# Kernel optimization log

Measured on AMD Instinct MI355X. Metric: run time of the kernel, lower is better.

The kernel has to match this reference:

```python
import jax, jax.numpy as jnp
import numpy as np

B = 4096          # trees (characters)
T = 16            # nodes per tree template
VC, VO = 2000, 16
D, H = 256, 512


def _build_trees(rng):
    # template: perfect binary tree depth 3 (nodes 0..14, leaves 7..14) + extra leaf 15
    # node 3 is ternary with third child 15
    left_t = np.full(T, -1, np.int32)
    right_t = np.full(T, -1, np.int32)
    third_t = np.full(T, -1, np.int32)
    for i in range(7):
        left_t[i] = 2 * i + 1
        right_t[i] = 2 * i + 2
    third_t[3] = 15
    off = (np.arange(B, dtype=np.int32) * T)[:, None]
    def shift(t):
        return np.where(t[None, :] >= 0, t[None, :] + off, -1).ravel().astype(np.int32)
    left, right, third = shift(left_t), shift(right_t), shift(third_t)
    comp = np.zeros((B, T), np.int32)
    comp[:, 7:] = rng.integers(1, VC, size=(B, 9))      # leaves get real components
    op = np.zeros((B, T), np.int32)
    op[:, :7] = rng.integers(1, VO, size=(B, 7))        # internal nodes get operators
    lvl0 = (off + np.array([0])).ravel().astype(np.int32)
    lvl1 = (off + np.array([1, 2])).ravel().astype(np.int32)
    lvl2 = (off + np.array([3, 4, 5, 6])).ravel().astype(np.int32)
    return comp.ravel(), op.ravel(), left, right, third, lvl2, lvl1, lvl0


def setup_inputs() -> dict:
    rng = np.random.default_rng(0)
    comp, op, left, right, third, lvl2, lvl1, lvl0 = _build_trees(rng)
    def xavier(fi, fo):
        s = np.sqrt(6.0 / (fi + fo))
        return jnp.asarray(rng.uniform(-s, s, size=(fi, fo)).astype(np.float32))
    comp_table = rng.normal(0, 0.02, size=(VC, D)).astype(np.float32)
    comp_table[0] = 0.0  # padding_idx
    op_table = rng.normal(0, 0.02, size=(VO, D)).astype(np.float32)
    op_table[0] = 0.0
    return {
        'component_ids': jnp.asarray(comp), 'operator_ids': jnp.asarray(op),
        'left_child': jnp.asarray(left), 'right_child': jnp.asarray(right),
        'third_child': jnp.asarray(third),
        'lvl2_idx': jnp.asarray(lvl2), 'lvl1_idx': jnp.asarray(lvl1), 'lvl0_idx': jnp.asarray(lvl0),
        'comp_table': jnp.asarray(comp_table), 'op_table': jnp.asarray(op_table),
        'W1b': xavier(3 * D, H), 'b1b': jnp.zeros((H,), jnp.float32),
        'W2b': xavier(H, D), 'b2b': jnp.zeros((D,), jnp.float32),
        'W1t': xavier(4 * D, H), 'b1t': jnp.zeros((H,), jnp.float32),
        'W2t': xavier(H, D), 'b2t': jnp.zeros((D,), jnp.float32),
        'gamma': jnp.ones((D,), jnp.float32), 'beta': jnp.zeros((D,), jnp.float32),
    }


def _ln(x, gamma, beta, eps=1e-5):
    mu = jnp.mean(x, axis=-1, keepdims=True)
    var = jnp.mean(jnp.square(x - mu), axis=-1, keepdims=True)
    return (x - mu) * jax.lax.rsqrt(var + eps) * gamma + beta


def reference(component_ids, operator_ids, left_child, right_child, third_child,
              lvl2_idx, lvl1_idx, lvl0_idx,
              comp_table, op_table, W1b, b1b, W2b, b2b, W1t, b1t, W2t, b2t,
              gamma, beta):
    node_embeds = comp_table[component_ids]               # [N, D]
    for idx in (lvl2_idx, lvl1_idx, lvl0_idx):            # bottom-up levels
        op_e = op_table[operator_ids[idx]]                # [L, D]
        le = node_embeds[left_child[idx]]
        re = node_embeds[right_child[idx]]
        ti = third_child[idx]
        has3 = (ti >= 0)
        te = node_embeds[jnp.maximum(ti, 0)] * has3[:, None].astype(node_embeds.dtype)
        b_in = jnp.concatenate([op_e, le, re], axis=-1)   # [L, 3D]
        b_out = jax.nn.gelu(b_in @ W1b + b1b, approximate=False) @ W2b + b2b
        t_in = jnp.concatenate([op_e, le, re, te], axis=-1)  # [L, 4D]
        t_out = jax.nn.gelu(t_in @ W1t + b1t, approximate=False) @ W2t + b2t
        new_b = _ln(b_out + le + re, gamma, beta)
        new_t = _ln(t_out + (le + re + te) / 3.0, gamma, beta)
        new = jnp.where(has3[:, None], new_t, new_b)
        node_embeds = node_embeds.at[idx].set(new)
    return node_embeds[lvl0_idx]                          # [B, D] root embeddings (eval: no dropout)
```

## Files before the change

### kernel.cpp

```cpp
#include <hip/hip_runtime.h>

typedef __bf16 bf16_t;
typedef __attribute__((ext_vector_type(8))) __bf16 bf16x8;
typedef __attribute__((ext_vector_type(4))) __bf16 bf16x4;
typedef __attribute__((ext_vector_type(4))) float f32x4;

#define GLL16(gsrc, ldst) __builtin_amdgcn_global_load_lds( \
    (const __attribute__((address_space(1))) void*)(gsrc),  \
    (__attribute__((address_space(3))) void*)(ldst), 16, 0, 0)
#define SBAR() __builtin_amdgcn_s_barrier()
#define SCHED0() __builtin_amdgcn_sched_barrier(0)

__global__ void detect_dtype(const unsigned short* __restrict__ ct, int* __restrict__ flag) {
    if (threadIdx.x == 0 && blockIdx.x == 0) {
        int ok = 1;
        for (int i = 0; i < 16; i++) {
            int e = (ct[256 + i] >> 7) & 0xFF;
            ok &= (e >= 80 && e <= 126) ? 1 : 0;
        }
        *flag = ok;
    }
}

__global__ void prep(const void* __restrict__ op_table, bf16_t* __restrict__ opb,
                     const void* __restrict__ comp_table, bf16_t* __restrict__ ctb,
                     const void* __restrict__ W1b, bf16_t* __restrict__ W1bp,
                     const void* __restrict__ W1t, bf16_t* __restrict__ W1tp,
                     const void* __restrict__ W2b, bf16_t* __restrict__ W2bp,
                     const void* __restrict__ W2t, bf16_t* __restrict__ W2tp,
                     const int* __restrict__ flagp,
                     const int* __restrict__ lvl2, const int* __restrict__ lvl1,
                     const int* __restrict__ lvl0, const int* __restrict__ third,
                     int* __restrict__ lists, int* __restrict__ cnts,
                     int* __restrict__ inv) {
    int b = blockIdx.x, tid = threadIdx.x;
    if (b >= 6624) {
        int r = (b - 6624) * 256 + tid;
        int slot, lr, base_t, base_b;
        const int* lvl;
        if (r < 16384)      { slot = 0; lr = r;         lvl = lvl2; base_t = 0;     base_b = 16384; }
        else if (r < 24576) { slot = 1; lr = r - 16384; lvl = lvl1; base_t = 32768; base_b = 40960; }
        else                { slot = 2; lr = r - 24576; lvl = lvl0; base_t = 49152; base_b = 53248; }
        int node = lvl[lr];
        int tern = third[node] >= 0 ? 1 : 0;
        if (slot == 0)      inv[node] = lr;
        else if (slot == 1) inv[node] = 16384 + lr;

        unsigned long long bt = __ballot(tern);
        unsigned long long bb = __ballot(!tern);
        int lane = tid & 63;
        unsigned long long ltm = (1ull << lane) - 1ull;
        int post = __popcll(bt & ltm), posb = __popcll(bb & ltm);
        int baseT = 0, baseB = 0;
        if (lane == 0) {
            baseT = atomicAdd(&cnts[slot * 2 + 1], __popcll(bt));
            baseB = atomicAdd(&cnts[slot * 2 + 0], __popcll(bb));
        }
        baseT = __shfl(baseT, 0, 64);
        baseB = __shfl(baseB, 0, 64);
        lists[tern ? (base_t + baseT + post) : (base_b + baseB + posb)] = lr;
        return;
    }
    int isbf = *flagp;
    if (b < 16) {
        int i = b * 256 + tid;
        opb[i] = isbf ? ((const bf16_t*)op_table)[i] : (bf16_t)((const float*)op_table)[i];
        return;
    }
    if (b < 2016) {
        int i = (b - 16) * 256 + tid;
        ctb[i] = isbf ? ((const bf16_t*)comp_table)[i] : (bf16_t)((const float*)comp_table)[i];
        return;
    }
    const void* src; bf16_t* dst; int e0, Nmask, Nshift;
    if (b < 3552)      { src = W1b; dst = W1bp; e0 = (b - 2016) * 256; Nmask = 511; Nshift = 9; }
    else if (b < 5600) { src = W1t; dst = W1tp; e0 = (b - 3552) * 256; Nmask = 511; Nshift = 9; }
    else if (b < 6112) { src = W2b; dst = W2bp; e0 = (b - 5600) * 256; Nmask = 255; Nshift = 8; }
    else               { src = W2t; dst = W2tp; e0 = (b - 6112) * 256; Nmask = 255; Nshift = 8; }
    int e = e0 + tid;
    bf16_t v = isbf ? ((const bf16_t*)src)[e] : (bf16_t)((const float*)src)[e];
    int n = e & Nmask, k = e >> Nshift;
    int kc = k >> 5, kl = k & 31;
    int gp = (kl >> 3) ^ ((n >> 1) & 3);
    dst[(size_t)(((kc << Nshift) + n) << 5) + (gp << 3) + (kl & 7)] = v;
}

__device__ __forceinline__ void load8f(const bf16_t* ne2, const void* ct, int isbf,
                                       int invn, int cidn, int q, float* o) {
    if (invn >= 0) {
        bf16x8 v = *(const bf16x8*)(ne2 + (size_t)invn * 256 + q);
        for (int z = 0; z < 8; z++) o[z] = (float)v[z];
    } else if (isbf) {
        bf16x8 v = *(const bf16x8*)((const bf16_t*)ct + (size_t)cidn * 256 + q);
        for (int z = 0; z < 8; z++) o[z] = (float)v[z];
    } else {
        const float* fp = (const float*)ct + (size_t)cidn * 256 + q;
        f32x4 a = *(const f32x4*)fp, b = *(const f32x4*)(fp + 4);
        for (int z = 0; z < 4; z++) { o[z] = a[z]; o[z + 4] = b[z]; }
    }
}

__device__ __forceinline__ float ldparam(const void* p, int i, int isbf) {
    return isbf ? (float)((const bf16_t*)p)[i] : ((const float*)p)[i];
}

__global__ __launch_bounds__(512, 4) void fused_level(
    const int* __restrict__ list_t, const int* __restrict__ list_b,
    const int* __restrict__ cntpair, const int* __restrict__ lvl_idx,
    const int* __restrict__ op_ids, const int* __restrict__ lch,
    const int* __restrict__ rch, const int* __restrict__ tch,
    bf16_t* __restrict__ ne2, const bf16_t* __restrict__ opb,
    const void* __restrict__ ct, const bf16_t* __restrict__ ctb,
    const int* __restrict__ cid, const int* __restrict__ inv,
    const int* __restrict__ flagp,
    const bf16_t* __restrict__ W1tp, const void* __restrict__ b1t,
    const bf16_t* __restrict__ W2tp, const void* __restrict__ b2t,
    const bf16_t* __restrict__ W1bp, const void* __restrict__ b1b,
    const bf16_t* __restrict__ W2bp, const void* __restrict__ b2b,
    const void* __restrict__ gma, const void* __restrict__ bta,
    int slotBase, void* __restrict__ out)
{
    __shared__ __align__(1024) char smem[69632];

    const int tid = threadIdx.x;
    const int w = tid >> 6, lane = tid & 63, cc = lane & 15, qq = lane >> 4;
    const int gx = (cc >> 1) & 3;
    const int e7 = cc & 7;
    const int cnt_t = cntpair[1], cnt_b = cntpair[0];
    const int blocks_t = (cnt_t + 31) >> 5;
    int tern, base, cnt, K1c;
    const int* list;
    const bf16_t *W1p, *W2p;
    const void *b1, *b2;
    if ((int)blockIdx.x < blocks_t) {
        tern = 1; list = list_t; base = blockIdx.x * 32; cnt = cnt_t;
        W1p = W1tp; b1 = b1t; W2p = W2tp; b2 = b2t; K1c = 32;
    } else {
        tern = 0; list = list_b; base = (blockIdx.x - blocks_t) * 32; cnt = cnt_b;
        if (base >= cnt) return;
        W1p = W1bp; b1 = b1b; W2p = W2bp; b2 = b2b; K1c = 24;
    }
    const int act = min(32, cnt - base);
    const int isbf = *flagp;

    int glA = 0, opSA = 0;
    int aInv0 = 0, aInv1 = 0, aInv2 = 0, aCid0 = 0, aCid1 = 0, aCid2 = 0;
    if (tid < 128) {
        int rowA = tid >> 2;
        glA = (tid & 3) ^ ((rowA >> 1) & 3);
        int rA = list[base + min(rowA, act - 1)];
        int nA = lvl_idx[rA];
        opSA = op_ids[nA];
        int a0 = lch[nA], a1 = rch[nA];
        int a2 = tern ? tch[nA] : a0;
        aInv0 = inv[a0]; aInv1 = inv[a1]; aInv2 = inv[a2];
        aCid0 = aInv0 < 0 ? cid[a0] : 0;
        aCid1 = aInv1 < 0 ? cid[a1] : 0;
        aCid2 = aInv2 < 0 ? cid[a2] : 0;
    }

    const int ms = tid >> 4, gs = tid & 15;
    const int lr = list[base + min(ms, act - 1)];
    const int node = lvl_idx[lr];
    const int c0 = lch[node], c1 = rch[node];
    const int c2 = tern ? tch[node] : c0;
    int sInv[3] = {inv[c0], inv[c1], inv[c2]};
    int sCid[3];
    sCid[0] = sInv[0] < 0 ? cid[c0] : 0;
    sCid[1] = sInv[1] < 0 ? cid[c1] : 0;
    sCid[2] = sInv[2] < 0 ? cid[c2] : 0;

    float b2f[2], gf[2], btf[2];
    for (int j = 0; j < 2; j++) {
        int col = (w + 8 * j) * 16 + cc;
        b2f[j] = ldparam(b2, col, isbf);
        gf[j] = ldparam(gma, col, isbf);
        btf[j] = ldparam(bta, col, isbf);
    }

    const f32x4 zf = {0.f, 0.f, 0.f, 0.f};
    f32x4 acc1[2][4];
    for (int m = 0; m < 2; m++) for (int j = 0; j < 4; j++) acc1[m][j] = zf;

#define STAGE1(kc_, bsel_) do {                                                   \
        const char* srcb_ = (const char*)W1p + ((size_t)(kc_) << 15);             \
        char* dstb_ = smem + ((bsel_) << 15);                                     \
        _Pragma("unroll")                                                         \
        for (int i_ = 0; i_ < 4; i_++) {                                          \
            int off_ = ((i_ << 3) + w) << 10;                                     \
            GLL16(srcb_ + off_ + (lane << 4), dstb_ + off_);                      \
        }                                                                         \
        if (w < 2) {                                                              \
            int colg_ = (kc_) * 32 + glA * 8;                                     \
            int piece_ = colg_ >> 8, po_ = colg_ & 255;                           \
            int iv_ = piece_ == 1 ? aInv0 : piece_ == 2 ? aInv1 : aInv2;          \
            int cd_ = piece_ == 1 ? aCid0 : piece_ == 2 ? aCid1 : aCid2;          \
            const bf16_t* s_ = piece_ == 0 ? opb + (size_t)opSA * 256             \
                : (iv_ >= 0 ? ne2 + (size_t)iv_ * 256 : ctb + (size_t)cd_ * 256); \
            GLL16(s_ + po_, smem + 65536 + ((bsel_) << 11) + (w << 10));          \
        }                                                                         \
    } while (0)

    STAGE1(0, 0);
    for (int kc = 0; kc < K1c; kc++) {
        const int cur = kc & 1;
        const bool more = kc + 1 < K1c;
        if (more) STAGE1(kc + 1, cur ^ 1);
        if (more) {
            if (w < 2) asm volatile("s_waitcnt vmcnt(5)" ::: "memory");
            else       asm volatile("s_waitcnt vmcnt(4)" ::: "memory");
        } else {
            asm volatile("s_waitcnt vmcnt(0)" ::: "memory");
        }
        SCHED0();
        SBAR();
        SCHED0();
        const bf16_t* as = (const bf16_t*)(smem + 65536 + (cur << 11));
        const bf16_t* bs = (const bf16_t*)(smem + (cur << 15));
        bf16x8 af[2];
        for (int m = 0; m < 2; m++)
            af[m] = *(const bf16x8*)(as + (m * 16 + cc) * 32 + ((qq ^ gx) << 3));
        __builtin_amdgcn_s_setprio(1);
        for (int j = 0; j < 4; j++) {
            bf16x8 bv = *(const bf16x8*)(bs + ((w + 8 * j) * 16 + cc) * 32 + ((qq ^ gx) << 3));
            for (int m = 0; m < 2; m++)
                acc1[m][j] = __builtin_amdgcn_mfma_f32_16x16x32_bf16(bv, af[m], acc1[m][j], 0, 0, 0);
        }
        __builtin_amdgcn_s_setprio(0);
        SCHED0();
        SBAR();
    }

#define STAGE2(kc_, bsel_) do {                                                   \
        const char* srcb_ = (const char*)W2p + ((size_t)(kc_) << 14);             \
        char* dstb_ = smem + ((bsel_) << 14);                                     \
        _Pragma("unroll")                                                         \
        for (int i_ = 0; i_ < 2; i_++) {                                          \
            int off_ = ((i_ << 3) + w) << 10;                                     \
            GLL16(srcb_ + off_ + (lane << 4), dstb_ + off_);                      \
        }                                                                         \
    } while (0)

    STAGE2(0, 0);
    {
        unsigned short* Hs = (unsigned short*)(smem + 32768);
        for (int j = 0; j < 4; j++) {
            float b1q[4];
            for (int r = 0; r < 4; r++) b1q[r] = ldparam(b1, (w + 8 * j) * 16 + qq * 4 + r, isbf);
            int c16 = ((w + 8 * j) << 1) + (qq >> 1);
            for (int m = 0; m < 2; m++) {
                int row = m * 16 + cc;
                bf16x4 hv;
                for (int r = 0; r < 4; r++) {
                    float v = acc1[m][j][r] + b1q[r];
                    hv[r] = (bf16_t)(0.5f * v * (1.0f + erff(v * 0.70710678118654752f)));
                }
                *(bf16x4*)(Hs + (row << 9) + ((c16 ^ e7) << 3) + ((qq & 1) << 2)) = hv;
            }
        }
    }

    f32x4 acc2[2][2];
    for (int m = 0; m < 2; m++) for (int j = 0; j < 2; j++) acc2[m][j] = zf;
    for (int kc = 0; kc < 16; kc++) {
        const int cur = kc & 1;
        const bool more = kc + 1 < 16;
        if (more) STAGE2(kc + 1, cur ^ 1);
        if (more) asm volatile("s_waitcnt vmcnt(2) lgkmcnt(0)" ::: "memory");
        else      asm volatile("s_waitcnt vmcnt(0) lgkmcnt(0)" ::: "memory");
        SCHED0();
        SBAR();
        SCHED0();
        const unsigned short* Hs = (const unsigned short*)(smem + 32768);
        const bf16_t* bs = (const bf16_t*)(smem + (cur << 14));
        bf16x8 af[2];
        for (int m = 0; m < 2; m++)
            af[m] = *(const bf16x8*)(Hs + ((m * 16 + cc) << 9) + ((((kc << 2) + qq) ^ e7) << 3));
        __builtin_amdgcn_s_setprio(1);
        for (int j = 0; j < 2; j++) {
            bf16x8 bv = *(const bf16x8*)(bs + ((w + 8 * j) * 16 + cc) * 32 + ((qq ^ gx) << 3));
            for (int m = 0; m < 2; m++)
                acc2[m][j] = __builtin_amdgcn_mfma_f32_16x16x32_bf16(af[m], bv, acc2[m][j], 0, 0, 0);
        }
        __builtin_amdgcn_s_setprio(0);
        SCHED0();
        SBAR();
    }
    __syncthreads();

    {
        float* Rf = (float*)smem;
        int colb = gs * 16;
        for (int i = 0; i < 2; i++) {
            int q = colb + i * 8;
            float lv[8], rv[8], tv[8];
            load8f(ne2, ct, isbf, sInv[0], sCid[0], q, lv);
            load8f(ne2, ct, isbf, sInv[1], sCid[1], q, rv);
            if (tern) load8f(ne2, ct, isbf, sInv[2], sCid[2], q, tv);
            f32x4 s0, s1;
            if (tern) {
                for (int z = 0; z < 4; z++) {
                    s0[z] = (lv[z] + rv[z] + tv[z]) * (1.0f / 3.0f);
                    s1[z] = (lv[z + 4] + rv[z + 4] + tv[z + 4]) * (1.0f / 3.0f);
                }
            } else {
                for (int z = 0; z < 4; z++) {
                    s0[z] = lv[z] + rv[z];
                    s1[z] = lv[z + 4] + rv[z + 4];
                }
            }
            *(f32x4*)(Rf + ms * 256 + q) = s0;
            *(f32x4*)(Rf + ms * 256 + q + 4) = s1;
        }
    }
    __syncthreads();

    float* partS = (float*)(smem + 65536);
    float* partQ = partS + 256;
    float* muA   = partQ + 256;
    float* rsA   = muA + 32;
    const float* Rf = (const float*)smem;

    for (int m = 0; m < 2; m++) for (int r = 0; r < 4; r++) {
        int row = m * 16 + qq * 4 + r;
        float ps = 0.f, pq = 0.f;
        for (int j = 0; j < 2; j++) {
            int col = (w + 8 * j) * 16 + cc;
            float x = acc2[m][j][r] + b2f[j] + Rf[(row << 8) + col];
            acc2[m][j][r] = x;
            ps += x; pq += x * x;
        }
        for (int d = 1; d < 16; d <<= 1) {
            ps += __shfl_xor(ps, d, 64);
            pq += __shfl_xor(pq, d, 64);
        }
        if (cc == 0) { partS[w * 32 + row] = ps; partQ[w * 32 + row] = pq; }
    }
    __syncthreads();
    if (tid < 32) {
        float s = 0.f, sq = 0.f;
        for (int i = 0; i < 8; i++) {
            s  += partS[i * 32 + tid];
            sq += partQ[i * 32 + tid];
        }
        float mu = s * (1.0f / 256.0f);
        float var = sq * (1.0f / 256.0f) - mu * mu;
        muA[tid] = mu;
        rsA[tid] = rsqrtf(fmaxf(var, 0.0f) + 1e-5f);
    }
    __syncthreads();

    for (int m = 0; m < 2; m++) for (int r = 0; r < 4; r++) {
        int row = m * 16 + qq * 4 + r;
        if (row >= act) continue;
        float mu = muA[row], rs = rsA[row];
        int lr2 = list[base + row];
        for (int j = 0; j < 2; j++) {
            int col = (w + 8 * j) * 16 + cc;
            float y = (acc2[m][j][r] - mu) * rs * gf[j] + btf[j];
            if (out) {
                if (isbf) ((bf16_t*)out)[(size_t)lr2 * 256 + col] = (bf16_t)y;
                else      ((float*)out)[(size_t)lr2 * 256 + col] = y;
            } else {
                ne2[(size_t)(slotBase + lr2) * 256 + col] = (bf16_t)y;
            }
        }
    }
#undef STAGE1
#undef STAGE2
}

extern "C" void kernel_launch(void* const* d_in, const int* in_sizes, int n_in,
                              void* d_out, int out_size, void* d_ws, size_t ws_size,
                              hipStream_t stream) {
    const int* cid    = (const int*)d_in[0];
    const int* opids  = (const int*)d_in[1];
    const int* lch    = (const int*)d_in[2];
    const int* rch    = (const int*)d_in[3];
    const int* tch    = (const int*)d_in[4];
    const int* lvl2   = (const int*)d_in[5];
    const int* lvl1   = (const int*)d_in[6];
    const int* lvl0   = (const int*)d_in[7];
    const void* comp_table = d_in[8];
    const void* op_table   = d_in[9];
    const void* W1b = d_in[10];
    const void* b1b = d_in[11];
    const void* W2b = d_in[12];
    const void* b2b = d_in[13];
    const void* W1t = d_in[14];
    const void* b1t = d_in[15];
    const void* W2t = d_in[16];
    const void* b2t = d_in[17];
    const void* gma = d_in[18];
    const void* bta = d_in[19];

    char* wsp = (char*)d_ws;
    bf16_t* ne2  = (bf16_t*)wsp;                 size_t off = 12582912;
    bf16_t* opb  = (bf16_t*)(wsp + off);         off += 8192;
    bf16_t* ctb  = (bf16_t*)(wsp + off);         off += 1024000;
    bf16_t* W1bp = (bf16_t*)(wsp + off);         off += 786432;
    bf16_t* W1tp = (bf16_t*)(wsp + off);         off += 1048576;
    bf16_t* W2bp = (bf16_t*)(wsp + off);         off += 262144;
    bf16_t* W2tp = (bf16_t*)(wsp + off);         off += 262144;
    int* inv   = (int*)(wsp + off);              off += 262144;
    int* lists = (int*)(wsp + off);              off += 229376;
    int* cnts  = (int*)(wsp + off);              off += 64;
    int* flag  = cnts + 8;

    hipMemsetAsync(cnts, 0, 64, stream);
    hipMemsetAsync(inv, 0xFF, 262144, stream);
    detect_dtype<<<1, 64, 0, stream>>>((const unsigned short*)comp_table, flag);
    prep<<<6736, 256, 0, stream>>>(op_table, opb, comp_table, ctb,
                                   W1b, W1bp, W1t, W1tp, W2b, W2bp, W2t, W2tp, flag,
                                   lvl2, lvl1, lvl0, tch, lists, cnts, inv);

    fused_level<<<513, 512, 0, stream>>>(lists + 0, lists + 16384, cnts + 0, lvl2,
        opids, lch, rch, tch, ne2, opb, comp_table, ctb, cid, inv, flag,
        W1tp, b1t, W2tp, b2t, W1bp, b1b, W2bp, b2b, gma, bta, 0, nullptr);
    fused_level<<<257, 512, 0, stream>>>(lists + 32768, lists + 40960, cnts + 2, lvl1,
        opids, lch, rch, tch, ne2, opb, comp_table, ctb, cid, inv, flag,
        W1tp, b1t, W2tp, b2t, W1bp, b1b, W2bp, b2b, gma, bta, 16384, nullptr);
    fused_level<<<129, 512, 0, stream>>>(lists + 49152, lists + 53248, cnts + 4, lvl0,
        opids, lch, rch, tch, ne2, opb, comp_table, ctb, cid, inv, flag,
        W1tp, b1t, W2tp, b2t, W1bp, b1b, W2bp, b2b, gma, bta, 0, d_out);
}
```

Before: 216.9 us.

## Stage weights per-wave in LDS and load activations directly to remove block barriers

Each wave now stages only its own slice of W1/W2 into a private LDS region, laid out unswizzled, so the main GEMM loops need no block-wide barriers. Activation fragments are read straight from global memory into registers instead of being staged through shared LDS. The launch-bounds occupancy hint is lowered from 4 to 2 and LDS shrinks slightly. The intent is to cut barrier stalls and LDS traffic, at the cost of more direct global loads, possible LDS bank conflicts without the swizzle, and redundant prefetches at loop ends.

```diff
diff --git a/kernel.cpp b/kernel.cpp
--- a/kernel.cpp
+++ b/kernel.cpp
@@ -80,9 +80,7 @@
     int e = e0 + tid;
     bf16_t v = isbf ? ((const bf16_t*)src)[e] : (bf16_t)((const float*)src)[e];
     int n = e & Nmask, k = e >> Nshift;
-    int kc = k >> 5, kl = k & 31;
-    int gp = (kl >> 3) ^ ((n >> 1) & 3);
-    dst[(size_t)(((kc << Nshift) + n) << 5) + (gp << 3) + (kl & 7)] = v;
+    dst[(size_t)((((k >> 5) << Nshift) + n) * 32 + (k & 31))] = v;
 }
 
 __device__ __forceinline__ void load8f(const bf16_t* ne2, const void* ct, int isbf,
@@ -104,7 +102,7 @@
     return isbf ? (float)((const bf16_t*)p)[i] : ((const float*)p)[i];
 }
 
-__global__ __launch_bounds__(512, 4) void fused_level(
+__global__ __launch_bounds__(512, 2) void fused_level(
     const int* __restrict__ list_t, const int* __restrict__ list_b,
     const int* __restrict__ cntpair, const int* __restrict__ lvl_idx,
     const int* __restrict__ op_ids, const int* __restrict__ lch,
@@ -120,11 +118,10 @@
     const void* __restrict__ gma, const void* __restrict__ bta,
     int slotBase, void* __restrict__ out)
 {
-    __shared__ __align__(1024) char smem[69632];
+    __shared__ __align__(1024) char smem[68096];
 
     const int tid = threadIdx.x;
     const int w = tid >> 6, lane = tid & 63, cc = lane & 15, qq = lane >> 4;
-    const int gx = (cc >> 1) & 3;
     const int e7 = cc & 7;
     const int cnt_t = cntpair[1], cnt_b = cntpair[0];
     const int blocks_t = (cnt_t + 31) >> 5;
@@ -143,20 +140,27 @@
     const int act = min(32, cnt - base);
     const int isbf = *flagp;
 
-    int glA = 0, opSA = 0;
-    int aInv0 = 0, aInv1 = 0, aInv2 = 0, aCid0 = 0, aCid1 = 0, aCid2 = 0;
-    if (tid < 128) {
-        int rowA = tid >> 2;
-        glA = (tid & 3) ^ ((rowA >> 1) & 3);
-        int rA = list[base + min(rowA, act - 1)];
-        int nA = lvl_idx[rA];
-        opSA = op_ids[nA];
-        int a0 = lch[nA], a1 = rch[nA];
-        int a2 = tern ? tch[nA] : a0;
-        aInv0 = inv[a0]; aInv1 = inv[a1]; aInv2 = inv[a2];
-        aCid0 = aInv0 < 0 ? cid[a0] : 0;
-        aCid1 = aInv1 < 0 ? cid[a1] : 0;
-        aCid2 = aInv2 < 0 ? cid[a2] : 0;
+    const bf16_t *a0p0, *a0p1, *a0p2, *a0p3, *a1p0, *a1p1, *a1p2, *a1p3;
+    {
+        int r0 = cc, r1 = 16 + cc;
+        int lr0 = list[base + min(r0, act - 1)];
+        int nd0 = lvl_idx[lr0];
+        a0p0 = opb + (size_t)op_ids[nd0] * 256;
+        int x0 = lch[nd0], x1 = rch[nd0];
+        int x2 = tern ? tch[nd0] : x0;
+        int i0 = inv[x0], i1 = inv[x1], i2 = inv[x2];
+        a0p1 = i0 >= 0 ? ne2 + (size_t)i0 * 256 : ctb + (size_t)cid[x0] * 256;
+        a0p2 = i1 >= 0 ? ne2 + (size_t)i1 * 256 : ctb + (size_t)cid[x1] * 256;
+        a0p3 = i2 >= 0 ? ne2 + (size_t)i2 * 256 : ctb + (size_t)cid[x2] * 256;
+        int lr1 = list[base + min(r1, act - 1)];
+        int nd1 = lvl_idx[lr1];
+        a1p0 = opb + (size_t)op_ids[nd1] * 256;
+        int y0 = lch[nd1], y1 = rch[nd1];
+        int y2 = tern ? tch[nd1] : y0;
+        int j0 = inv[y0], j1 = inv[y1], j2 = inv[y2];
+        a1p1 = j0 >= 0 ? ne2 + (size_t)j0 * 256 : ctb + (size_t)cid[y0] * 256;
+        a1p2 = j1 >= 0 ? ne2 + (size_t)j1 * 256 : ctb + (size_t)cid[y1] * 256;
+        a1p3 = j2 >= 0 ? ne2 + (size_t)j2 * 256 : ctb + (size_t)cid[y2] * 256;
     }
 
     const int ms = tid >> 4, gs = tid & 15;
@@ -178,72 +182,83 @@
         btf[j] = ldparam(bta, col, isbf);
     }
 
+    const int nrowB1 = (w + 8 * (lane >> 4)) * 16 + (lane & 15);
+    const int r2 = lane & 31;
+    const int nrowB2 = (w + 8 * (r2 >> 4)) * 16 + (r2 & 15);
+    const int i2base = lane >> 5;
+
+#define STAGE1(kc_, sel_) do {                                                     \
+        const char* s_ = (const char*)W1p + ((size_t)(kc_) << 15) + nrowB1 * 64;   \
+        char* d_ = smem + (w << 13) + ((sel_) << 12);                              \
+        GLL16(s_,      d_);                                                        \
+        GLL16(s_ + 16, d_ + 1024);                                                 \
+        GLL16(s_ + 32, d_ + 2048);                                                 \
+        GLL16(s_ + 48, d_ + 3072);                                                 \
+    } while (0)
+#define STAGE2(kc_, sel_) do {                                                     \
+        const char* s_ = (const char*)W2p + ((size_t)(kc_) << 14)                  \
+                         + nrowB2 * 64 + i2base * 16;                              \
+        char* d_ = smem + 32768 + (w << 12) + ((sel_) << 11);                      \
+        GLL16(s_,      d_);                                                        \
+        GLL16(s_ + 32, d_ + 1024);                                                 \
+    } while (0)
+#define AFLOAD(kc_, f0_, f1_) do {                                                 \
+        int colg_ = (kc_) * 32 + qq * 8;                                           \
+        int piece_ = colg_ >> 8, po_ = colg_ & 255;                                \
+        const bf16_t* s0_ = piece_ == 0 ? a0p0 : piece_ == 1 ? a0p1                \
+                          : piece_ == 2 ? a0p2 : a0p3;                             \
+        const bf16_t* s1_ = piece_ == 0 ? a1p0 : piece_ == 1 ? a1p1                \
+                          : piece_ == 2 ? a1p2 : a1p3;                             \
+        f0_ = *(const bf16x8*)(s0_ + po_);                                         \
+        f1_ = *(const bf16x8*)(s1_ + po_);                                         \
+    } while (0)
+
     const f32x4 zf = {0.f, 0.f, 0.f, 0.f};
     f32x4 acc1[2][4];
     for (int m = 0; m < 2; m++) for (int j = 0; j < 4; j++) acc1[m][j] = zf;
 
-#define STAGE1(kc_, bsel_) do {                                                   \
-        const char* srcb_ = (const char*)W1p + ((size_t)(kc_) << 15);             \
-        char* dstb_ = smem + ((bsel_) << 15);                                     \
-        _Pragma("unroll")                                                         \
-        for (int i_ = 0; i_ < 4; i_++) {                                          \
-            int off_ = ((i_ << 3) + w) << 10;                                     \
-            GLL16(srcb_ + off_ + (lane << 4), dstb_ + off_);                      \
-        }                                                                         \
-        if (w < 2) {                                                              \
-            int colg_ = (kc_) * 32 + glA * 8;                                     \
-            int piece_ = colg_ >> 8, po_ = colg_ & 255;                           \
-            int iv_ = piece_ == 1 ? aInv0 : piece_ == 2 ? aInv1 : aInv2;          \
-            int cd_ = piece_ == 1 ? aCid0 : piece_ == 2 ? aCid1 : aCid2;          \
-            const bf16_t* s_ = piece_ == 0 ? opb + (size_t)opSA * 256             \
-                : (iv_ >= 0 ? ne2 + (size_t)iv_ * 256 : ctb + (size_t)cd_ * 256); \
-            GLL16(s_ + po_, smem + 65536 + ((bsel_) << 11) + (w << 10));          \
-        }                                                                         \
-    } while (0)
-
+    bf16x8 afA0, afA1, afB0, afB1;
     STAGE1(0, 0);
-    for (int kc = 0; kc < K1c; kc++) {
-        const int cur = kc & 1;
-        const bool more = kc + 1 < K1c;
-        if (more) STAGE1(kc + 1, cur ^ 1);
-        if (more) {
-            if (w < 2) asm volatile("s_waitcnt vmcnt(5)" ::: "memory");
-            else       asm volatile("s_waitcnt vmcnt(4)" ::: "memory");
-        } else {
-            asm volatile("s_waitcnt vmcnt(0)" ::: "memory");
-        }
-        SCHED0();
-        SBAR();
-        SCHED0();
-        const bf16_t* as = (const bf16_t*)(smem + 65536 + (cur << 11));
-        const bf16_t* bs = (const bf16_t*)(smem + (cur << 15));
-        bf16x8 af[2];
-        for (int m = 0; m < 2; m++)
-            af[m] = *(const bf16x8*)(as + (m * 16 + cc) * 32 + ((qq ^ gx) << 3));
-        __builtin_amdgcn_s_setprio(1);
-        for (int j = 0; j < 4; j++) {
-            bf16x8 bv = *(const bf16x8*)(bs + ((w + 8 * j) * 16 + cc) * 32 + ((qq ^ gx) << 3));
-            for (int m = 0; m < 2; m++)
-                acc1[m][j] = __builtin_amdgcn_mfma_f32_16x16x32_bf16(bv, af[m], acc1[m][j], 0, 0, 0);
-        }
-        __builtin_amdgcn_s_setprio(0);
-        SCHED0();
-        SBAR();
-    }
-
-#define STAGE2(kc_, bsel_) do {                                                   \
-        const char* srcb_ = (const char*)W2p + ((size_t)(kc_) << 14);             \
-        char* dstb_ = smem + ((bsel_) << 14);                                     \
-        _Pragma("unroll")                                                         \
-        for (int i_ = 0; i_ < 2; i_++) {                                          \
-            int off_ = ((i_ << 3) + w) << 10;                                     \
-            GLL16(srcb_ + off_ + (lane << 4), dstb_ + off_);                      \
-        }                                                                         \
-    } while (0)
+    AFLOAD(0, afA0, afA1);
+    for (int kc = 0; kc < K1c; kc += 2) {
+        {
+            int kn = kc + 1 < K1c ? kc + 1 : K1c - 1;
+            STAGE1(kn, 1);
+            AFLOAD(kn, afB0, afB1);
+            asm volatile("s_waitcnt vmcnt(6)" ::: "memory");
+            SCHED0();
+            const char* bs = smem + (w << 13);
+            __builtin_amdgcn_s_setprio(1);
+            for (int j = 0; j < 4; j++) {
+                bf16x8 bv = *(const bf16x8*)(bs + (qq << 10) + ((j * 16 + cc) << 4));
+                acc1[0][j] = __builtin_amdgcn_mfma_f32_16x16x32_bf16(bv, afA0, acc1[0][j], 0, 0, 0);
+                acc1[1][j] = __builtin_amdgcn_mfma_f32_16x16x32_bf16(bv, afA1, acc1[1][j], 0, 0, 0);
+            }
+            __builtin_amdgcn_s_setprio(0);
+        }
+        {
+            int kn = kc + 2 < K1c ? kc + 2 : K1c - 1;
+            STAGE1(kn, 0);
+            AFLOAD(kn, afA0, afA1);
+            asm volatile("s_waitcnt vmcnt(6)" ::: "memory");
+            SCHED0();
+            const char* bs = smem + (w << 13) + 4096;
+            __builtin_amdgcn_s_setprio(1);
+            for (int j = 0; j < 4; j++) {
+                bf16x8 bv = *(const bf16x8*)(bs + (qq << 10) + ((j * 16 + cc) << 4));
+                acc1[0][j] = __builtin_amdgcn_mfma_f32_16x16x32_bf16(bv, afB0, acc1[0][j], 0, 0, 0);
+                acc1[1][j] = __builtin_amdgcn_mfma_f32_16x16x32_bf16(bv, afB1, acc1[1][j], 0, 0, 0);
+            }
+            __builtin_amdgcn_s_setprio(0);
+        }
+    }
+    asm volatile("s_waitcnt vmcnt(0)" ::: "memory");
+    SCHED0();
+    SBAR();
 
     STAGE2(0, 0);
     {
-        unsigned short* Hs = (unsigned short*)(smem + 32768);
+        unsigned short* Hs = (unsigned short*)smem;
         for (int j = 0; j < 4; j++) {
             float b1q[4];
             for (int r = 0; r < 4; r++) b1q[r] = ldparam(b1, (w + 8 * j) * 16 + qq * 4 + r, isbf);
@@ -259,33 +274,32 @@
             }
         }
     }
+    asm volatile("s_waitcnt vmcnt(0) lgkmcnt(0)" ::: "memory");
+    SCHED0();
+    SBAR();
 
     f32x4 acc2[2][2];
     for (int m = 0; m < 2; m++) for (int j = 0; j < 2; j++) acc2[m][j] = zf;
     for (int kc = 0; kc < 16; kc++) {
-        const int cur = kc & 1;
-        const bool more = kc + 1 < 16;
-        if (more) STAGE2(kc + 1, cur ^ 1);
-        if (more) asm volatile("s_waitcnt vmcnt(2) lgkmcnt(0)" ::: "memory");
-        else      asm volatile("s_waitcnt vmcnt(0) lgkmcnt(0)" ::: "memory");
+        const int sel = kc & 1;
+        const int kn = kc + 1 < 16 ? kc + 1 : 15;
+        STAGE2(kn, sel ^ 1);
+        asm volatile("s_waitcnt vmcnt(2)" ::: "memory");
         SCHED0();
-        SBAR();
-        SCHED0();
-        const unsigned short* Hs = (const unsigned short*)(smem + 32768);
-        const bf16_t* bs = (const bf16_t*)(smem + (cur << 14));
+        const unsigned short* Hs = (const unsigned short*)smem;
+        const char* b2s = smem + 32768 + (w << 12) + (sel << 11);
         bf16x8 af[2];
         for (int m = 0; m < 2; m++)
             af[m] = *(const bf16x8*)(Hs + ((m * 16 + cc) << 9) + ((((kc << 2) + qq) ^ e7) << 3));
         __builtin_amdgcn_s_setprio(1);
         for (int j = 0; j < 2; j++) {
-            bf16x8 bv = *(const bf16x8*)(bs + ((w + 8 * j) * 16 + cc) * 32 + ((qq ^ gx) << 3));
+            bf16x8 bv = *(const bf16x8*)(b2s + (qq << 9) + ((j * 16 + cc) << 4));
             for (int m = 0; m < 2; m++)
                 acc2[m][j] = __builtin_amdgcn_mfma_f32_16x16x32_bf16(af[m], bv, acc2[m][j], 0, 0, 0);
         }
         __builtin_amdgcn_s_setprio(0);
-        SCHED0();
-        SBAR();
-    }
+    }
+    asm volatile("s_waitcnt vmcnt(0)" ::: "memory");
     __syncthreads();
 
     {
@@ -368,6 +382,7 @@
     }
 #undef STAGE1
 #undef STAGE2
+#undef AFLOAD
 }
 
 extern "C" void kernel_launch(void* const* d_in, const int* in_sizes, int n_in,
```

New measurement: 284.5 us. 31.2% more time.
